# Kernel optimization log

Hardware: AMD Instinct MI355X
Metric: run time of the kernel (lower is better)

## Reference

```python
import jax, jax.numpy as jnp
import numpy as np

N_NODES = 100000
N_EDGES = 1600000
IN_C, HID_C, OUT_C, N_CLS = 128, 128, 128, 40


def setup_inputs() -> dict:
    key = jax.random.key(0)
    ks = jax.random.split(key, 10)
    x = jax.random.normal(ks[0], (N_NODES, IN_C), dtype=jnp.float32)
    edge_index = jax.random.randint(ks[1], (2, N_EDGES), 0, N_NODES, dtype=jnp.int64)
    s = 1.0 / np.sqrt(IN_C)
    W_self1 = jax.random.uniform(ks[2], (IN_C, HID_C), jnp.float32, -s, s)
    W_neigh1 = jax.random.uniform(ks[3], (IN_C, HID_C), jnp.float32, -s, s)
    b1 = jnp.zeros((HID_C,), jnp.float32)
    s2 = 1.0 / np.sqrt(HID_C)
    W_self2 = jax.random.uniform(ks[4], (HID_C, OUT_C), jnp.float32, -s2, s2)
    W_neigh2 = jax.random.uniform(ks[5], (HID_C, OUT_C), jnp.float32, -s2, s2)
    b2 = jnp.zeros((OUT_C,), jnp.float32)
    s3 = 1.0 / np.sqrt(OUT_C)
    W_cls = jax.random.uniform(ks[6], (OUT_C, N_CLS), jnp.float32, -s3, s3)
    b_cls = jax.random.uniform(ks[7], (N_CLS,), jnp.float32, -s3, s3)
    return dict(x=x, edge_index=edge_index, W_self1=W_self1, W_neigh1=W_neigh1, b1=b1,
                W_self2=W_self2, W_neigh2=W_neigh2, b2=b2, W_cls=W_cls, b_cls=b_cls)


def _mean_agg(h, src, dst, n_nodes):
    # sum of in-neighbor features per destination node, then divide by in-degree
    sums = jax.ops.segment_sum(h[src], dst, num_segments=n_nodes)  # [N, F]
    deg = jax.ops.segment_sum(jnp.ones(src.shape[0], h.dtype), dst, num_segments=n_nodes)
    return sums / jnp.maximum(deg, 1.0)[:, None]


def _sage_conv(h, src, dst, W_self, W_neigh, b):
    # DGL mean SAGEConv: fc_self(h) + fc_neigh(mean_neigh(h)) + bias
    h_neigh = _mean_agg(h, src, dst, h.shape[0])
    return h @ W_self + h_neigh @ W_neigh + b


def reference(x, edge_index, W_self1, W_neigh1, b1, W_self2, W_neigh2, b2, W_cls, b_cls):
    src, dst = edge_index[0], edge_index[1]
    h = jax.nn.relu(_sage_conv(x, src, dst, W_self1, W_neigh1, b1))
    h = jax.nn.relu(_sage_conv(h, src, dst, W_self2, W_neigh2, b2))
    return h @ W_cls + b_cls
```

## Files before the change

kernel.cpp:

```cpp
#include <hip/hip_runtime.h>

#define N_NODES 100000
#define N_EDGES 1600000
#define C 128
#define NCLS 40
#define NBUCK 196
#define BCAP 12288
#define NT_TILES 3125

typedef _Float16 half8 __attribute__((ext_vector_type(8)));
typedef float f32x4 __attribute__((ext_vector_type(4)));
typedef float f32x16 __attribute__((ext_vector_type(16)));


__global__ __launch_bounds__(256) void bucket_scatter_k(const int* __restrict__ src,
    const int* __restrict__ dst, int* __restrict__ bucket_cnt, int* __restrict__ bucketArr) {
  __shared__ int lh[NBUCK], lbase[NBUCK], lcur[NBUCK];
  int tid = threadIdx.x;
  for (int i = tid; i < NBUCK; i += 256) { lh[i] = 0; lcur[i] = 0; }
  __syncthreads();
  int base = blockIdx.x * 4096;
  int bmax = min(base + 4096, N_EDGES);
  for (int e = base + tid; e < bmax; e += 256)
    atomicAdd(&lh[dst[e] >> 9], 1);
  __syncthreads();
  for (int i = tid; i < NBUCK; i += 256)
    lbase[i] = lh[i] ? atomicAdd(&bucket_cnt[i], lh[i]) : 0;
  __syncthreads();
  for (int e = base + tid; e < bmax; e += 256) {
    int d = dst[e];
    int b = d >> 9, loc = d & 511;
    int p = lbase[b] + atomicAdd(&lcur[b], 1);
    if (p < BCAP) bucketArr[(size_t)b * BCAP + p] = (src[e] << 9) | loc;
  }
}

__global__ void bucket_scan_k(const int* __restrict__ bucket_cnt, int* __restrict__ bucket_base,
                              int* __restrict__ rp) {
  if (threadIdx.x == 0 && blockIdx.x == 0) {
    int run = 0;
    for (int b = 0; b < NBUCK; b++) {
      bucket_base[b] = run;
      run += min(bucket_cnt[b], BCAP);
    }
    bucket_base[NBUCK] = run;
    rp[N_NODES] = run;
  }
}

__global__ __launch_bounds__(256) void bucket_sort_k(const int* __restrict__ bucketArr,
    const int* __restrict__ bucket_cnt, const int* __restrict__ bucket_base,
    int* __restrict__ rp, int* __restrict__ csr) {
  __shared__ int hist[512], offs[512], curs[512];
  __shared__ int wpart[4];
  __shared__ int lsrc[BCAP];
  int b = blockIdx.x, tid = threadIdx.x;
  int cnt = min(bucket_cnt[b], BCAP);
  int base = bucket_base[b];
  for (int i = tid; i < 512; i += 256) hist[i] = 0;
  __syncthreads();
  for (int i = tid; i < cnt; i += 256)
    atomicAdd(&hist[bucketArr[(size_t)b * BCAP + i] & 511], 1);
  __syncthreads();
  int a0 = hist[2 * tid], a1 = hist[2 * tid + 1];
  int s = a0 + a1;
  int lane = tid & 63, wid = tid >> 6;
  int inc = s;
  for (int d = 1; d < 64; d <<= 1) { int y = __shfl_up(inc, d, 64); if (lane >= d) inc += y; }
  if (lane == 63) wpart[wid] = inc;
  __syncthreads();
  int woff = 0;
  for (int q = 0; q < wid; q++) woff += wpart[q];
  int ex = woff + inc - s;
  offs[2 * tid] = ex; offs[2 * tid + 1] = ex + a0;
  curs[2 * tid] = ex; curs[2 * tid + 1] = ex + a0;
  __syncthreads();
  for (int i = tid; i < 512; i += 256) {
    int gn = b * 512 + i;
    if (gn < N_NODES) rp[gn] = base + offs[i];
  }
  for (int i = tid; i < cnt; i += 256) {
    int packed = bucketArr[(size_t)b * BCAP + i];
    int p = atomicAdd(&curs[packed & 511], 1);
    lsrc[p] = packed >> 9;
  }
  __syncthreads();
  for (int i = tid; i < cnt; i += 256) csr[base + i] = lsrc[i];
}


__global__ __launch_bounds__(256) void f32_to_f16_k(const float* __restrict__ in,
                                                    _Float16* __restrict__ out) {
  int i = blockIdx.x * 256 + threadIdx.x;
  float4 v0 = *(const float4*)(in + (size_t)i * 8);
  float4 v1 = *(const float4*)(in + (size_t)i * 8 + 4);
  half8 o;
  o[0] = (_Float16)v0.x; o[1] = (_Float16)v0.y; o[2] = (_Float16)v0.z; o[3] = (_Float16)v0.w;
  o[4] = (_Float16)v1.x; o[5] = (_Float16)v1.y; o[6] = (_Float16)v1.z; o[7] = (_Float16)v1.w;
  *(half8*)(out + (size_t)i * 8) = o;
}

__global__ void build_wt_k(const float* __restrict__ Ws, const float* __restrict__ Wn,
                           _Float16* __restrict__ WT) {
  int n = blockIdx.x, k = threadIdx.x;
  float v = (k < 128) ? Ws[k * 128 + n] : Wn[(k - 128) * 128 + n];
  WT[n * 256 + k] = (_Float16)v;
}

__global__ void build_wct_k(const float* __restrict__ Wc, const float* __restrict__ bc,
                            _Float16* __restrict__ WcT, float* __restrict__ bcf) {
  int c = blockIdx.x, k = threadIdx.x;
  float v = (c < NCLS) ? Wc[k * NCLS + c] : 0.f;
  WcT[c * C + k] = (_Float16)v;
  if (k == 0) bcf[c] = (c < NCLS) ? bc[c] : 0.f;
}


__global__ __launch_bounds__(256) void agg_mean_h_k(const _Float16* __restrict__ feat,
    const int* __restrict__ rp, const int* __restrict__ csr, _Float16* __restrict__ out) {
  int w = threadIdx.x >> 6;
  int node = blockIdx.x * 4 + w;
  int lane = threadIdx.x & 63;
  int g = lane >> 4, lr = lane & 15;
  int beg = rp[node], end = rp[node + 1];
  float acc[8] = {}, acc2[8] = {};
  int j = beg;
  for (; j + 8 <= end; j += 8) {
    int e0 = csr[j + g];
    int e1 = csr[j + 4 + g];
    half8 v0 = *(const half8*)(feat + (size_t)e0 * C + lr * 8);
    half8 v1 = *(const half8*)(feat + (size_t)e1 * C + lr * 8);
#pragma unroll
    for (int q = 0; q < 8; q++) { acc[q] += (float)v0[q]; acc2[q] += (float)v1[q]; }
  }
  for (; j + 4 <= end; j += 4) {
    int e0 = csr[j + g];
    half8 v0 = *(const half8*)(feat + (size_t)e0 * C + lr * 8);
#pragma unroll
    for (int q = 0; q < 8; q++) acc[q] += (float)v0[q];
  }
  int rem = end - j;
  if (g < rem) {
    int e0 = csr[j + g];
    half8 v0 = *(const half8*)(feat + (size_t)e0 * C + lr * 8);
#pragma unroll
    for (int q = 0; q < 8; q++) acc2[q] += (float)v0[q];
  }
#pragma unroll
  for (int q = 0; q < 8; q++) {
    float v = acc[q] + acc2[q];
    v += __shfl_xor(v, 16, 64);
    v += __shfl_xor(v, 32, 64);
    acc[q] = v;
  }
  if (g == 0) {
    float inv = 1.0f / fmaxf((float)(end - beg), 1.0f);
    half8 o;
#pragma unroll
    for (int q = 0; q < 8; q++) o[q] = (_Float16)(acc[q] * inv);
    *(half8*)(out + (size_t)node * C + lr * 8) = o;
  }
}


__global__ __launch_bounds__(256) void sage_gemm_ws_k(
    const _Float16* __restrict__ Xs, const _Float16* __restrict__ Xn,
    const _Float16* __restrict__ WT, const float* __restrict__ bias,
    _Float16* __restrict__ out) {
  __shared__ _Float16 cbuf[32][136];
  int tid = threadIdx.x, lane = tid & 63, wid = tid >> 6;
  int l31 = lane & 31, l5 = lane >> 5;
  int col0 = wid * 32;

  half8 b[16];
#pragma unroll
  for (int ks = 0; ks < 16; ks++)
    b[ks] = *(const half8*)(WT + (size_t)(col0 + l31) * 256 + ks * 16 + l5 * 8);
  float bcol = bias[col0 + l31];

  for (int t = blockIdx.x; t < NT_TILES; t += gridDim.x) {
    size_t row0 = (size_t)t * 32;
    half8 a[16];
#pragma unroll
    for (int ks = 0; ks < 8; ks++) {
      a[ks]     = *(const half8*)(Xs + (row0 + l31) * C + ks * 16 + l5 * 8);
      a[ks + 8] = *(const half8*)(Xn + (row0 + l31) * C + ks * 16 + l5 * 8);
    }
    f32x16 acc = {};
#pragma unroll
    for (int ks = 0; ks < 16; ks++)
      acc = __builtin_amdgcn_mfma_f32_32x32x16_f16(a[ks], b[ks], acc, 0, 0, 0);

    __syncthreads();
#pragma unroll
    for (int q = 0; q < 16; q++) {
      int row = (q & 3) + 8 * (q >> 2) + 4 * l5;
      float v = fmaxf(acc[q] + bcol, 0.f);
      cbuf[row][col0 + l31] = (_Float16)v;
    }
    __syncthreads();
#pragma unroll
    for (int p = 0; p < 2; p++) {
      int chunk = tid + p * 256;
      int r = chunk >> 4, cg = chunk & 15;
      half8 v = *(const half8*)&cbuf[r][cg * 8];
      *(half8*)(out + (row0 + r) * C + cg * 8) = v;
    }
  }
}


__global__ __launch_bounds__(256) void classifier_mfma_k(const _Float16* __restrict__ h,
    const _Float16* __restrict__ WcT, const float* __restrict__ bcf, float* __restrict__ out) {
  __shared__ float cbuf[64][49];
  int tid = threadIdx.x, lane = tid & 63, wid = tid >> 6;
  int lr = lane & 15, lk = lane >> 4;
  int row0 = blockIdx.x * 64 + wid * 16;
  f32x4 acc[3] = {};
#pragma unroll
  for (int ks = 0; ks < 4; ks++) {
    half8 a = {};
    int r = row0 + lr;
    if (r < N_NODES) a = *(const half8*)(h + (size_t)r * C + ks * 32 + lk * 8);
#pragma unroll
    for (int nf = 0; nf < 3; nf++) {
      half8 bfr = *(const half8*)(WcT + (size_t)(nf * 16 + lr) * C + ks * 32 + lk * 8);
      acc[nf] = __builtin_amdgcn_mfma_f32_16x16x32_f16(a, bfr, acc[nf], 0, 0, 0);
    }
  }
#pragma unroll
  for (int nf = 0; nf < 3; nf++)
#pragma unroll
    for (int q = 0; q < 4; q++) {
      int c = nf * 16 + lr;
      cbuf[wid * 16 + lk * 4 + q][c] = acc[nf][q] + bcf[c];
    }
  __syncthreads();
  int row_blk0 = blockIdx.x * 64;
  for (int i = tid; i < 64 * NCLS; i += 256) {
    int r = i / NCLS, c = i - r * NCLS;
    int gr = row_blk0 + r;
    if (gr < N_NODES) out[(size_t)gr * NCLS + c] = cbuf[r][c];
  }
}


extern "C" void kernel_launch(void* const* d_in, const int* in_sizes, int n_in,
                              void* d_out, int out_size, void* d_ws, size_t ws_size,
                              hipStream_t stream) {
  (void)in_sizes; (void)n_in; (void)out_size; (void)ws_size;
  const float* x   = (const float*)d_in[0];
  const int*   ei  = (const int*)d_in[1];
  const float* Ws1 = (const float*)d_in[2];
  const float* Wn1 = (const float*)d_in[3];
  const float* b1  = (const float*)d_in[4];
  const float* Ws2 = (const float*)d_in[5];
  const float* Wn2 = (const float*)d_in[6];
  const float* b2  = (const float*)d_in[7];
  const float* Wc  = (const float*)d_in[8];
  const float* bc  = (const float*)d_in[9];
  const int* src = ei;
  const int* dst = ei + N_EDGES;

  char* ws = (char*)d_ws;
  size_t off = 0;
  auto alloc = [&](size_t bytes) {
    void* p = ws + off;
    off = (off + bytes + 255) & ~(size_t)255;
    return p;
  };
  int*      bucket_cnt  = (int*)alloc((size_t)NBUCK * 4);
  int*      bucket_base = (int*)alloc((size_t)(NBUCK + 1) * 4);
  int*      bucketArr   = (int*)alloc((size_t)NBUCK * BCAP * 4);
  int*      rp          = (int*)alloc((size_t)(N_NODES + 1) * 4);
  int*      csr         = (int*)alloc((size_t)N_EDGES * 4);
  _Float16* hA          = (_Float16*)alloc((size_t)N_NODES * C * 2);
  _Float16* hB          = (_Float16*)alloc((size_t)N_NODES * C * 2);
  _Float16* hC          = (_Float16*)alloc((size_t)N_NODES * C * 2);
  _Float16* WT1         = (_Float16*)alloc((size_t)C * 256 * 2);
  _Float16* WT2         = (_Float16*)alloc((size_t)C * 256 * 2);
  _Float16* WcT         = (_Float16*)alloc((size_t)48 * C * 2);
  float*    bcf         = (float*)alloc(48 * 4);
  float* outf = (float*)d_out;

  hipMemsetAsync(bucket_cnt, 0, (size_t)NBUCK * 4, stream);
  bucket_scatter_k<<<(N_EDGES + 4095) / 4096, 256, 0, stream>>>(src, dst, bucket_cnt, bucketArr);
  bucket_scan_k<<<1, 64, 0, stream>>>(bucket_cnt, bucket_base, rp);
  bucket_sort_k<<<NBUCK, 256, 0, stream>>>(bucketArr, bucket_cnt, bucket_base, rp, csr);

  build_wt_k<<<C, 256, 0, stream>>>(Ws1, Wn1, WT1);
  build_wt_k<<<C, 256, 0, stream>>>(Ws2, Wn2, WT2);
  build_wct_k<<<48, C, 0, stream>>>(Wc, bc, WcT, bcf);
  f32_to_f16_k<<<(N_NODES * C / 8) / 256, 256, 0, stream>>>(x, hA);

  agg_mean_h_k<<<N_NODES / 4, 256, 0, stream>>>(hA, rp, csr, hB);
  sage_gemm_ws_k<<<782, 256, 0, stream>>>(hA, hB, WT1, b1, hC);
  agg_mean_h_k<<<N_NODES / 4, 256, 0, stream>>>(hC, rp, csr, hB);
  sage_gemm_ws_k<<<782, 256, 0, stream>>>(hC, hB, WT2, b2, hA);
  classifier_mfma_k<<<(N_NODES + 63) / 64, 256, 0, stream>>>(hA, WcT, bcf, outf);
}
```

Measured before the change: 371.8 us.

## Fuse classifier into layer-2 GEMM, merge setup kernels, use fp16 accumulation in aggregation

Result: faster. 363.8 us (-2.2%).

```diff
diff --git a/kernel.cpp b/kernel.cpp
--- a/kernel.cpp
+++ b/kernel.cpp
@@ -21,42 +21,50 @@
   __syncthreads();
   int base = blockIdx.x * 4096;
   int bmax = min(base + 4096, N_EDGES);
-  for (int e = base + tid; e < bmax; e += 256)
-    atomicAdd(&lh[dst[e] >> 9], 1);
+  int dreg[16];
+  int nk = 0;
+  for (int e = base + tid; e < bmax; e += 256) dreg[nk++] = dst[e];
+  for (int k = 0; k < nk; k++) atomicAdd(&lh[dreg[k] >> 9], 1);
   __syncthreads();
   for (int i = tid; i < NBUCK; i += 256)
     lbase[i] = lh[i] ? atomicAdd(&bucket_cnt[i], lh[i]) : 0;
   __syncthreads();
+  nk = 0;
   for (int e = base + tid; e < bmax; e += 256) {
-    int d = dst[e];
+    int d = dreg[nk++];
     int b = d >> 9, loc = d & 511;
     int p = lbase[b] + atomicAdd(&lcur[b], 1);
     if (p < BCAP) bucketArr[(size_t)b * BCAP + p] = (src[e] << 9) | loc;
   }
 }
 
-__global__ void bucket_scan_k(const int* __restrict__ bucket_cnt, int* __restrict__ bucket_base,
-                              int* __restrict__ rp) {
-  if (threadIdx.x == 0 && blockIdx.x == 0) {
-    int run = 0;
-    for (int b = 0; b < NBUCK; b++) {
-      bucket_base[b] = run;
-      run += min(bucket_cnt[b], BCAP);
-    }
-    bucket_base[NBUCK] = run;
-    rp[N_NODES] = run;
-  }
-}
-
 __global__ __launch_bounds__(256) void bucket_sort_k(const int* __restrict__ bucketArr,
-    const int* __restrict__ bucket_cnt, const int* __restrict__ bucket_base,
-    int* __restrict__ rp, int* __restrict__ csr) {
+    const int* __restrict__ bucket_cnt, int* __restrict__ rp, int* __restrict__ csr) {
+  __shared__ int pref[NBUCK + 1];
   __shared__ int hist[512], offs[512], curs[512];
   __shared__ int wpart[4];
   __shared__ int lsrc[BCAP];
   int b = blockIdx.x, tid = threadIdx.x;
+  int lane = tid & 63, wid = tid >> 6;
+
+  {
+    int v = (tid < NBUCK) ? min(bucket_cnt[tid], BCAP) : 0;
+    int inc = v;
+    for (int d = 1; d < 64; d <<= 1) { int y = __shfl_up(inc, d, 64); if (lane >= d) inc += y; }
+    if (lane == 63) wpart[wid] = inc;
+    __syncthreads();
+    int woff = 0;
+    for (int q = 0; q < wid; q++) woff += wpart[q];
+    int ex = woff + inc - v;
+    if (tid < NBUCK) pref[tid] = ex;
+    if (tid == NBUCK - 1) pref[NBUCK] = ex + v;
+    __syncthreads();
+  }
+  int base = pref[b];
   int cnt = min(bucket_cnt[b], BCAP);
-  int base = bucket_base[b];
+  if (b == 0 && tid == 0) rp[N_NODES] = pref[NBUCK];
+  __syncthreads();
+
   for (int i = tid; i < 512; i += 256) hist[i] = 0;
   __syncthreads();
   for (int i = tid; i < cnt; i += 256)
@@ -64,7 +72,6 @@
   __syncthreads();
   int a0 = hist[2 * tid], a1 = hist[2 * tid + 1];
   int s = a0 + a1;
-  int lane = tid & 63, wid = tid >> 6;
   int inc = s;
   for (int d = 1; d < 64; d <<= 1) { int y = __shfl_up(inc, d, 64); if (lane >= d) inc += y; }
   if (lane == 63) wpart[wid] = inc;
@@ -100,19 +107,25 @@
   *(half8*)(out + (size_t)i * 8) = o;
 }
 
-__global__ void build_wt_k(const float* __restrict__ Ws, const float* __restrict__ Wn,
-                           _Float16* __restrict__ WT) {
-  int n = blockIdx.x, k = threadIdx.x;
-  float v = (k < 128) ? Ws[k * 128 + n] : Wn[(k - 128) * 128 + n];
-  WT[n * 256 + k] = (_Float16)v;
-}
-
-__global__ void build_wct_k(const float* __restrict__ Wc, const float* __restrict__ bc,
-                            _Float16* __restrict__ WcT, float* __restrict__ bcf) {
-  int c = blockIdx.x, k = threadIdx.x;
-  float v = (c < NCLS) ? Wc[k * NCLS + c] : 0.f;
-  WcT[c * C + k] = (_Float16)v;
-  if (k == 0) bcf[c] = (c < NCLS) ? bc[c] : 0.f;
+__global__ void build_weights_k(const float* __restrict__ Ws1, const float* __restrict__ Wn1,
+                                const float* __restrict__ Ws2, const float* __restrict__ Wn2,
+                                const float* __restrict__ Wc, const float* __restrict__ bc,
+                                _Float16* __restrict__ WT1, _Float16* __restrict__ WT2,
+                                _Float16* __restrict__ WcT, float* __restrict__ bcf) {
+  int b = blockIdx.x, k = threadIdx.x;
+  if (b < 128) {
+    float v = (k < 128) ? Ws1[k * 128 + b] : Wn1[(k - 128) * 128 + b];
+    WT1[b * 256 + k] = (_Float16)v;
+  } else if (b < 256) {
+    int n = b - 128;
+    float v = (k < 128) ? Ws2[k * 128 + n] : Wn2[(k - 128) * 128 + n];
+    WT2[n * 256 + k] = (_Float16)v;
+  } else if (k < 128) {
+    int c = b - 256;
+    float v = (c < NCLS) ? Wc[k * NCLS + c] : 0.f;
+    WcT[c * C + k] = (_Float16)v;
+    if (k == 0) bcf[c] = (c < NCLS) ? bc[c] : 0.f;
+  }
 }
 
 
@@ -123,32 +136,37 @@
   int lane = threadIdx.x & 63;
   int g = lane >> 4, lr = lane & 15;
   int beg = rp[node], end = rp[node + 1];
-  float acc[8] = {}, acc2[8] = {};
+  half8 h0 = {}, h1 = {}, h2 = {}, h3 = {};
   int j = beg;
-  for (; j + 8 <= end; j += 8) {
+  for (; j + 16 <= end; j += 16) {
     int e0 = csr[j + g];
     int e1 = csr[j + 4 + g];
+    int e2 = csr[j + 8 + g];
+    int e3 = csr[j + 12 + g];
     half8 v0 = *(const half8*)(feat + (size_t)e0 * C + lr * 8);
     half8 v1 = *(const half8*)(feat + (size_t)e1 * C + lr * 8);
-#pragma unroll
-    for (int q = 0; q < 8; q++) { acc[q] += (float)v0[q]; acc2[q] += (float)v1[q]; }
+    half8 v2 = *(const half8*)(feat + (size_t)e2 * C + lr * 8);
+    half8 v3 = *(const half8*)(feat + (size_t)e3 * C + lr * 8);
+    h0 += v0; h1 += v1; h2 += v2; h3 += v3;
   }
   for (; j + 4 <= end; j += 4) {
     int e0 = csr[j + g];
     half8 v0 = *(const half8*)(feat + (size_t)e0 * C + lr * 8);
-#pragma unroll
-    for (int q = 0; q < 8; q++) acc[q] += (float)v0[q];
+    h0 += v0;
   }
   int rem = end - j;
   if (g < rem) {
     int e0 = csr[j + g];
     half8 v0 = *(const half8*)(feat + (size_t)e0 * C + lr * 8);
-#pragma unroll
-    for (int q = 0; q < 8; q++) acc2[q] += (float)v0[q];
-  }
+    h1 += v0;
+  }
+  float acc[8];
+#pragma unroll
+  for (int q = 0; q < 8; q++)
+    acc[q] = ((float)h0[q] + (float)h1[q]) + ((float)h2[q] + (float)h3[q]);
 #pragma unroll
   for (int q = 0; q < 8; q++) {
-    float v = acc[q] + acc2[q];
+    float v = acc[q];
     v += __shfl_xor(v, 16, 64);
     v += __shfl_xor(v, 32, 64);
     acc[q] = v;
@@ -163,10 +181,12 @@
 }
 
 
+template <bool CLS>
 __global__ __launch_bounds__(256) void sage_gemm_ws_k(
     const _Float16* __restrict__ Xs, const _Float16* __restrict__ Xn,
     const _Float16* __restrict__ WT, const float* __restrict__ bias,
-    _Float16* __restrict__ out) {
+    const _Float16* __restrict__ WcT, const float* __restrict__ bcf,
+    _Float16* __restrict__ out_h, float* __restrict__ out_cls) {
   __shared__ _Float16 cbuf[32][136];
   int tid = threadIdx.x, lane = tid & 63, wid = tid >> 6;
   int l31 = lane & 31, l5 = lane >> 5;
@@ -199,48 +219,39 @@
       cbuf[row][col0 + l31] = (_Float16)v;
     }
     __syncthreads();
-#pragma unroll
-    for (int p = 0; p < 2; p++) {
-      int chunk = tid + p * 256;
-      int r = chunk >> 4, cg = chunk & 15;
-      half8 v = *(const half8*)&cbuf[r][cg * 8];
-      *(half8*)(out + (row0 + r) * C + cg * 8) = v;
+
+    if (!CLS) {
+#pragma unroll
+      for (int p = 0; p < 2; p++) {
+        int chunk = tid + p * 256;
+        int r = chunk >> 4, cg = chunk & 15;
+        half8 v = *(const half8*)&cbuf[r][cg * 8];
+        *(half8*)(out_h + (row0 + r) * C + cg * 8) = v;
+      }
+    } else if (wid < 2) {
+      int lr16 = lane & 15, lk = lane >> 4;
+      f32x4 cacc[3] = {};
+#pragma unroll
+      for (int ks = 0; ks < 4; ks++) {
+        half8 av = *(const half8*)(&cbuf[wid * 16 + lr16][ks * 32 + lk * 8]);
+#pragma unroll
+        for (int nf = 0; nf < 3; nf++) {
+          half8 bf = *(const half8*)(WcT + (size_t)(nf * 16 + lr16) * C + ks * 32 + lk * 8);
+          cacc[nf] = __builtin_amdgcn_mfma_f32_16x16x32_f16(av, bf, cacc[nf], 0, 0, 0);
+        }
+      }
+#pragma unroll
+      for (int nf = 0; nf < 3; nf++) {
+        int c = nf * 16 + lr16;
+        if (c < NCLS) {
+#pragma unroll
+          for (int q = 0; q < 4; q++) {
+            size_t r = row0 + wid * 16 + lk * 4 + q;
+            out_cls[r * NCLS + c] = cacc[nf][q] + bcf[c];
+          }
+        }
+      }
     }
-  }
-}
-
-
-__global__ __launch_bounds__(256) void classifier_mfma_k(const _Float16* __restrict__ h,
-    const _Float16* __restrict__ WcT, const float* __restrict__ bcf, float* __restrict__ out) {
-  __shared__ float cbuf[64][49];
-  int tid = threadIdx.x, lane = tid & 63, wid = tid >> 6;
-  int lr = lane & 15, lk = lane >> 4;
-  int row0 = blockIdx.x * 64 + wid * 16;
-  f32x4 acc[3] = {};
-#pragma unroll
-  for (int ks = 0; ks < 4; ks++) {
-    half8 a = {};
-    int r = row0 + lr;
-    if (r < N_NODES) a = *(const half8*)(h + (size_t)r * C + ks * 32 + lk * 8);
-#pragma unroll
-    for (int nf = 0; nf < 3; nf++) {
-      half8 bfr = *(const half8*)(WcT + (size_t)(nf * 16 + lr) * C + ks * 32 + lk * 8);
-      acc[nf] = __builtin_amdgcn_mfma_f32_16x16x32_f16(a, bfr, acc[nf], 0, 0, 0);
-    }
-  }
-#pragma unroll
-  for (int nf = 0; nf < 3; nf++)
-#pragma unroll
-    for (int q = 0; q < 4; q++) {
-      int c = nf * 16 + lr;
-      cbuf[wid * 16 + lk * 4 + q][c] = acc[nf][q] + bcf[c];
-    }
-  __syncthreads();
-  int row_blk0 = blockIdx.x * 64;
-  for (int i = tid; i < 64 * NCLS; i += 256) {
-    int r = i / NCLS, c = i - r * NCLS;
-    int gr = row_blk0 + r;
-    if (gr < N_NODES) out[(size_t)gr * NCLS + c] = cbuf[r][c];
   }
 }
 
@@ -270,7 +281,6 @@
     return p;
   };
   int*      bucket_cnt  = (int*)alloc((size_t)NBUCK * 4);
-  int*      bucket_base = (int*)alloc((size_t)(NBUCK + 1) * 4);
   int*      bucketArr   = (int*)alloc((size_t)NBUCK * BCAP * 4);
   int*      rp          = (int*)alloc((size_t)(N_NODES + 1) * 4);
   int*      csr         = (int*)alloc((size_t)N_EDGES * 4);
@@ -285,17 +295,13 @@
 
   hipMemsetAsync(bucket_cnt, 0, (size_t)NBUCK * 4, stream);
   bucket_scatter_k<<<(N_EDGES + 4095) / 4096, 256, 0, stream>>>(src, dst, bucket_cnt, bucketArr);
-  bucket_scan_k<<<1, 64, 0, stream>>>(bucket_cnt, bucket_base, rp);
-  bucket_sort_k<<<NBUCK, 256, 0, stream>>>(bucketArr, bucket_cnt, bucket_base, rp, csr);
-
-  build_wt_k<<<C, 256, 0, stream>>>(Ws1, Wn1, WT1);
-  build_wt_k<<<C, 256, 0, stream>>>(Ws2, Wn2, WT2);
-  build_wct_k<<<48, C, 0, stream>>>(Wc, bc, WcT, bcf);
+  bucket_sort_k<<<NBUCK, 256, 0, stream>>>(bucketArr, bucket_cnt, rp, csr);
+
+  build_weights_k<<<304, 256, 0, stream>>>(Ws1, Wn1, Ws2, Wn2, Wc, bc, WT1, WT2, WcT, bcf);
   f32_to_f16_k<<<(N_NODES * C / 8) / 256, 256, 0, stream>>>(x, hA);
 
   agg_mean_h_k<<<N_NODES / 4, 256, 0, stream>>>(hA, rp, csr, hB);
-  sage_gemm_ws_k<<<782, 256, 0, stream>>>(hA, hB, WT1, b1, hC);
+  sage_gemm_ws_k<false><<<782, 256, 0, stream>>>(hA, hB, WT1, b1, nullptr, nullptr, hC, nullptr);
   agg_mean_h_k<<<N_NODES / 4, 256, 0, stream>>>(hC, rp, csr, hB);
-  sage_gemm_ws_k<<<782, 256, 0, stream>>>(hC, hB, WT2, b2, hA);
-  classifier_mfma_k<<<(N_NODES + 63) / 64, 256, 0, stream>>>(hA, WcT, bcf, outf);
-}
+  sage_gemm_ws_k<true><<<782, 256, 0, stream>>>(hC, hB, WT2, b2, WcT, bcf, nullptr, outf);
+}
```
